# Optimization experiments

Measured on AMD Instinct MI355X. Metric: run time of the kernel, lower is better.

## Reference

```python
import jax, jax.numpy as jnp
import numpy as np

N_IN = 1024
N_OUT = 1024
N_SAMPLES = 64
BATCH = 4096
SIGMA_INITIAL = 0.1
MUMAX_INITIAL = 1.0


def setup_inputs() -> dict:
    key = jax.random.key(0)
    ks = jax.random.split(key, 5)
    lsig = jnp.float32(np.log(SIGMA_INITIAL))
    return {
        "x": jax.random.normal(ks[0], (BATCH, N_IN), dtype=jnp.float32),
        "w_mu": jax.random.uniform(ks[1], (N_OUT, N_IN), dtype=jnp.float32,
                                   minval=-MUMAX_INITIAL, maxval=MUMAX_INITIAL),
        "w_lsigma": jnp.full((N_OUT, N_IN), lsig, dtype=jnp.float32),
        "b_mu": jax.random.uniform(ks[2], (N_OUT,), dtype=jnp.float32,
                                   minval=-MUMAX_INITIAL, maxval=MUMAX_INITIAL),
        "b_lsigma": jnp.full((N_OUT,), lsig, dtype=jnp.float32),
        "r1": jax.random.normal(ks[3], (N_SAMPLES, N_OUT, N_IN), dtype=jnp.float32),
        "r2": jax.random.normal(ks[4], (N_SAMPLES, N_OUT), dtype=jnp.float32),
        "N_samples": N_SAMPLES,
    }


def reference(x, w_mu, w_lsigma, b_mu, b_lsigma, r1, r2, N_samples):
    # Reparameterized weight/bias samples: (S, N_out, N_in), (S, N_out)
    w = w_mu + jnp.exp(w_lsigma) * r1
    b = b_mu + jnp.exp(b_lsigma) * r2
    # y[s, b, o] = sum_i x[b, i] * w[s, o, i] + b[s, o]
    y = jnp.einsum('bi,soi->sbo', x, w) + b[:, None, :]
    return y
```

## Files before the change

### kernel.cpp

```cpp
#include <hip/hip_runtime.h>
#include <hip/hip_bf16.h>
#include <hip/hip_fp8.h>
#include <stdint.h>
#include <type_traits>

#define NIN  1024
#define NOUT 1024
#define NB   4096

typedef float f32x4  __attribute__((ext_vector_type(4)));
typedef float f32x16 __attribute__((ext_vector_type(16)));
typedef __bf16 bf16x8 __attribute__((ext_vector_type(8)));
typedef int   i32x4 __attribute__((ext_vector_type(4)));
typedef int   i32x8 __attribute__((ext_vector_type(8)));

typedef const __attribute__((address_space(1))) unsigned int* gp1_t;
typedef __attribute__((address_space(3))) unsigned int* lp3_t;

__device__ __forceinline__ void gload16(const void* g, void* l) {
    __builtin_amdgcn_global_load_lds((gp1_t)g, (lp3_t)l, 16, 0, 0);
}

__device__ __forceinline__ unsigned short f2bf(float f) {
    __bf16 h = (__bf16)f;
    return __builtin_bit_cast(unsigned short, h);
}

__device__ __forceinline__ unsigned int pk4_fp8(float a, float b, float c, float d) {
#if __has_builtin(__builtin_amdgcn_cvt_pk_fp8_f32)
    int p = __builtin_amdgcn_cvt_pk_fp8_f32(a, b, 0, false);
    p = __builtin_amdgcn_cvt_pk_fp8_f32(c, d, p, true);
    return (unsigned int)p;
#else
    __hip_fp8_e4m3 qa(a), qb(b), qc(c), qd(d);
    return (unsigned int)qa.__x | ((unsigned int)qb.__x << 8) |
           ((unsigned int)qc.__x << 16) | ((unsigned int)qd.__x << 24);
#endif
}

#define BAR   __builtin_amdgcn_s_barrier()
#define LGK0  do { asm volatile("s_waitcnt lgkmcnt(0)" ::: "memory"); __builtin_amdgcn_sched_barrier(0); } while (0)
#define VMW4  do { asm volatile("s_waitcnt vmcnt(4)"  ::: "memory"); __builtin_amdgcn_sched_barrier(0); } while (0)
#define VMW2  do { asm volatile("s_waitcnt vmcnt(2)"  ::: "memory"); __builtin_amdgcn_sched_barrier(0); } while (0)
#define VMW0  do { asm volatile("s_waitcnt vmcnt(0)"  ::: "memory"); __builtin_amdgcn_sched_barrier(0); } while (0)

__global__ void cvt_x_kernel(const float* __restrict__ x, unsigned short* __restrict__ xb) {
    int i = blockIdx.x * blockDim.x + threadIdx.x;
    f32x4 v = reinterpret_cast<const f32x4*>(x)[i];
    ushort4 o;
    o.x = f2bf(v.x); o.y = f2bf(v.y); o.z = f2bf(v.z); o.w = f2bf(v.w);
    reinterpret_cast<ushort4*>(xb)[i] = o;
}

__global__ void cvt_x_fp8(const float* __restrict__ x, unsigned int* __restrict__ xf8) {
    int i = blockIdx.x * blockDim.x + threadIdx.x;
    f32x4 v = reinterpret_cast<const f32x4*>(x)[i];
    xf8[i] = pk4_fp8(v.x, v.y, v.z, v.w);
}

__global__ void cvt_r1_fp8(const float* __restrict__ wls, const float* __restrict__ r1,
                           unsigned int* __restrict__ rf8, int s0) {
    int idx = blockIdx.x * blockDim.x + threadIdx.x;
    int i4 = idx & 262143;
    int c  = idx >> 18;
    f32x4 ls = reinterpret_cast<const f32x4*>(wls)[i4];
    const f32x4* rp = reinterpret_cast<const f32x4*>(r1 + ((size_t)(s0 + c) << 20));
    f32x4 r = __builtin_nontemporal_load(rp + i4);
    rf8[idx] = pk4_fp8(__expf(ls.x) * r.x, __expf(ls.y) * r.y,
                       __expf(ls.z) * r.z, __expf(ls.w) * r.w);
}

__global__ void bias_kernel(const float* __restrict__ bmu, const float* __restrict__ bls,
                            const float* __restrict__ r2, float* __restrict__ bias, int total) {
    int i = blockIdx.x * blockDim.x + threadIdx.x;
    if (i < total) {
        int o = i & (NOUT - 1);
        bias[i] = bmu[o] + __expf(bls[o]) * r2[i];
    }
}

__launch_bounds__(512, 2)
__global__ void gemm256(const unsigned short* __restrict__ xb,
                        const unsigned short* __restrict__ wb,
                        unsigned short* __restrict__ yb, int nwg) {
    __shared__ __align__(16) char smem[131072];
    const int tid = threadIdx.x;
    const int l   = tid & 63;
    const int w   = tid >> 6;
    const int wr  = w >> 2, wc = w & 3;

    const int b   = blockIdx.x;
    const int q8  = nwg >> 3;
    const int g   = (b & 7) * q8 + (b >> 3);
    const int mi  = g & 15;
    const int ni  = g >> 4;
    const int m0  = mi * 256;
    const int n0  = ni * 256;

    const int srow = l >> 3;
    const int scol = ((l & 7) ^ srow) * 8;
    const size_t slane = (size_t)srow * NIN + scol;

    const int rowp  = (l & 15) * 128;
    const int colp0 = ((l >> 4) ^ (l & 7)) << 4;

    f32x4 acc[8][4] = {};
    bf16x8 aF[4][2], b0F[2][2], b1F[2][2];

    const unsigned short* xbase = xb + (size_t)m0 * NIN;
    const unsigned short* wbase = wb + (size_t)n0 * NIN;

    auto STAGE = [&](int buf, int kt, int q) {
        const int R = (q & 3) * 64 + w * 8;
        const unsigned short* src = ((q < 4) ? xbase : wbase)
                                    + (size_t)R * NIN + kt * 64 + slane;
        char* dst = smem + buf * 65536 + ((q >= 4) ? 32768 : 0) + R * 128;
        gload16(src, dst);
    };
    auto LDA = [&](int buf, int mh) {
        const char* base = smem + buf * 65536 + (wr * 128 + mh * 64) * 128 + rowp;
        #pragma unroll
        for (int mb = 0; mb < 4; ++mb) {
            aF[mb][0] = *(const bf16x8*)(base + mb * 2048 + colp0);
            aF[mb][1] = *(const bf16x8*)(base + mb * 2048 + (colp0 ^ 64));
        }
    };
    auto LDB = [&](bf16x8 (&bF)[2][2], int buf, int nh) {
        const char* base = smem + buf * 65536 + 32768 + (wc * 64 + nh * 32) * 128 + rowp;
        #pragma unroll
        for (int nb = 0; nb < 2; ++nb) {
            bF[nb][0] = *(const bf16x8*)(base + nb * 2048 + colp0);
            bF[nb][1] = *(const bf16x8*)(base + nb * 2048 + (colp0 ^ 64));
        }
    };
    auto MM = [&](auto MHc, auto NHc, bf16x8 (&bF)[2][2]) {
        constexpr int MH = decltype(MHc)::value;
        constexpr int NH = decltype(NHc)::value;
        __builtin_amdgcn_s_setprio(1);
        #pragma unroll
        for (int mb = 0; mb < 4; ++mb)
            #pragma unroll
            for (int nb = 0; nb < 2; ++nb)
                #pragma unroll
                for (int kk = 0; kk < 2; ++kk)
                    acc[MH * 4 + mb][NH * 2 + nb] = __builtin_amdgcn_mfma_f32_16x16x32_bf16(
                        aF[mb][kk], bF[nb][kk], acc[MH * 4 + mb][NH * 2 + nb], 0, 0, 0);
        __builtin_amdgcn_s_setprio(0);
    };

    auto C0 = std::integral_constant<int, 0>{};
    auto C1 = std::integral_constant<int, 1>{};

    auto ITER = [&](auto LASTc, int t1, int t2, int t3) {
        constexpr bool LAST = decltype(LASTc)::value;
        LDA(0, 0); LDB(b0F, 0, 0);
        STAGE(1, t1, 2); STAGE(1, t1, 3);
        BAR; LGK0; MM(C0, C0, b0F); BAR;
        LDB(b1F, 0, 1);
        STAGE(1, t1, 4); STAGE(1, t1, 5);
        BAR; LGK0; MM(C0, C1, b1F); BAR;
        LDA(0, 1);
        STAGE(1, t1, 6); STAGE(1, t1, 7);
        BAR; LGK0; MM(C1, C1, b1F); BAR;
        if constexpr (!LAST) { STAGE(0, t2, 0); STAGE(0, t2, 1); }
        BAR; MM(C1, C0, b0F);
        if constexpr (LAST) { VMW0; } else { VMW2; }
        BAR;
        LDA(1, 0); LDB(b0F, 1, 0);
        if constexpr (!LAST) { STAGE(0, t2, 2); STAGE(0, t2, 3); }
        BAR; LGK0; MM(C0, C0, b0F); BAR;
        LDB(b1F, 1, 1);
        if constexpr (!LAST) { STAGE(0, t2, 4); STAGE(0, t2, 5); }
        BAR; LGK0; MM(C0, C1, b1F); BAR;
        LDA(1, 1);
        if constexpr (!LAST) { STAGE(0, t2, 6); STAGE(0, t2, 7); }
        BAR; LGK0; MM(C1, C1, b1F); BAR;
        if constexpr (!LAST) {
            STAGE(1, t3, 0); STAGE(1, t3, 1);
            BAR; MM(C1, C0, b0F); VMW2; BAR;
        } else {
            MM(C1, C0, b0F);
        }
    };

    #pragma unroll
    for (int q = 0; q < 8; ++q) STAGE(0, 0, q);
    STAGE(1, 1, 0); STAGE(1, 1, 1);
    VMW2; BAR;

    #pragma unroll 1
    for (int i = 0; i < 7; ++i)
        ITER(std::false_type{}, 2 * i + 1, 2 * i + 2, 2 * i + 3);
    ITER(std::true_type{}, 15, 16, 17);

    const int oc = n0 + wc * 64 + (l & 15);
    #pragma unroll
    for (int mb = 0; mb < 8; ++mb) {
        #pragma unroll
        for (int i2 = 0; i2 < 4; ++i2) {
            int row = m0 + wr * 128 + mb * 16 + (l >> 4) * 4 + i2;
            unsigned short* rp = yb + (size_t)row * NOUT + oc;
            #pragma unroll
            for (int nb = 0; nb < 4; ++nb)
                rp[nb * 16] = f2bf(acc[mb][nb][i2]);
        }
    }
}

__launch_bounds__(512, 4)
__global__ void gemm_mx(const unsigned char* __restrict__ xf8,
                        const unsigned char* __restrict__ rf8,
                        const unsigned short* __restrict__ y0b,
                        const float* __restrict__ bias,
                        float* __restrict__ out, int s0, int nwg) {
    __shared__ __align__(16) char smem[65536];
    const int tid = threadIdx.x;
    const int l   = tid & 63;
    const int w   = tid >> 6;
    const int wr  = w >> 1, wc = w & 1;

    const int b   = blockIdx.x;
    const int q8  = nwg >> 3;
    const int g   = (b & 7) * q8 + (b >> 3);
    const int nni = nwg >> 5;
    const int mi  = g / nni;
    const int ni  = g - mi * nni;
    const int m0  = mi * 128;
    const int n0  = ni * 128;

    const int srow  = l >> 3;
    const size_t slane = (size_t)srow * NIN + ((l & 7) ^ srow) * 16;

    const int arow = l & 31;
    const int swz  = l & 7;
    const int kx   = (l >> 5) * 2;

    f32x16 acc[2] = {};
    i32x8 aF[2], bF[2][2];

    const unsigned char* xbase = xf8 + (size_t)m0 * NIN;
    const unsigned char* rbase = rf8 + (size_t)n0 * NIN;

    auto STAGE4 = [&](int buf, int t) {
        char* base = smem + buf * 32768;
        #pragma unroll
        for (int q = 0; q < 2; ++q) {
            const int R0 = q * 64 + w * 8;
            gload16(xbase + (size_t)R0 * NIN + t * 128 + slane, base + R0 * 128);
        }
        #pragma unroll
        for (int q = 0; q < 2; ++q) {
            const int R0 = q * 64 + w * 8;
            gload16(rbase + (size_t)R0 * NIN + t * 128 + slane, base + 16384 + R0 * 128);
        }
    };

    auto LDFRAGS = [&](int buf) {
        const char* Ab = smem + buf * 32768;
        const char* rbA = Ab + (wr * 32 + arow) * 128;
        #pragma unroll
        for (int ks = 0; ks < 2; ++ks) {
            int c = ks * 4 + kx;
            i32x4 lo = *(const i32x4*)(rbA + ((c ^ swz) * 16));
            i32x4 hi = *(const i32x4*)(rbA + (((c + 1) ^ swz) * 16));
            aF[ks] = __builtin_shufflevector(lo, hi, 0, 1, 2, 3, 4, 5, 6, 7);
        }
        #pragma unroll
        for (int nb = 0; nb < 2; ++nb) {
            const char* rbB = Ab + 16384 + (wc * 64 + nb * 32 + arow) * 128;
            #pragma unroll
            for (int ks = 0; ks < 2; ++ks) {
                int c = ks * 4 + kx;
                i32x4 lo = *(const i32x4*)(rbB + ((c ^ swz) * 16));
                i32x4 hi = *(const i32x4*)(rbB + (((c + 1) ^ swz) * 16));
                bF[nb][ks] = __builtin_shufflevector(lo, hi, 0, 1, 2, 3, 4, 5, 6, 7);
            }
        }
    };

    STAGE4(0, 0); STAGE4(1, 1);
    VMW4; BAR;

    #pragma unroll 1
    for (int t = 0; t < 8; ++t) {
        const int buf = t & 1;
        LDFRAGS(buf);
        LGK0;
        __builtin_amdgcn_s_setprio(1);
        #pragma unroll
        for (int nb = 0; nb < 2; ++nb)
            #pragma unroll
            for (int ks = 0; ks < 2; ++ks)
                acc[nb] = __builtin_amdgcn_mfma_scale_f32_32x32x64_f8f6f4(
                    aF[ks], bF[nb][ks], acc[nb],
                    0, 0, 0, 127, 0, 127);
        __builtin_amdgcn_s_setprio(0);
        BAR;
        if (t < 6)       { STAGE4(buf, t + 2); VMW4; BAR; }
        else if (t == 6) { VMW0; BAR; }
    }

    BAR;
    const int s   = s0 + (n0 >> 10);
    const int n0c = n0 & 1023;
    float* outp = out + (size_t)s * NB * NOUT;
    float* lds_f = (float*)smem;
    const f32x4 bvv = *(const f32x4*)(bias + (size_t)s * NOUT + n0c + (l & 31) * 4);

    #pragma unroll
    for (int nb = 0; nb < 2; ++nb) {
        const int col = wc * 64 + nb * 32 + (l & 31);
        #pragma unroll
        for (int r = 0; r < 16; ++r) {
            int row = wr * 32 + 4 * (l >> 5) + (r & 3) + 8 * (r >> 2);
            lds_f[row * 128 + col] = acc[nb][r];
        }
    }
    LGK0; BAR;
    #pragma unroll
    for (int k = 0; k < 8; ++k) {
        const int rl  = k * 16 + (tid >> 5);
        const int row = m0 + rl;
        f32x4 v = *(const f32x4*)(lds_f + rl * 128 + (l & 31) * 4);
        ushort4 yu = *(const ushort4*)(y0b + (size_t)row * NOUT + n0c + (l & 31) * 4);
        f32x4 yv;
        yv.x = __builtin_bit_cast(float, (unsigned int)yu.x << 16);
        yv.y = __builtin_bit_cast(float, (unsigned int)yu.y << 16);
        yv.z = __builtin_bit_cast(float, (unsigned int)yu.z << 16);
        yv.w = __builtin_bit_cast(float, (unsigned int)yu.w << 16);
        f32x4 o = v + yv + bvv;
        __builtin_nontemporal_store(o, (f32x4*)(outp + (size_t)row * NOUT + n0c + (l & 31) * 4));
    }
}

__global__ void fused_fallback(const float* __restrict__ x, const float* __restrict__ wmu,
                               const float* __restrict__ wls, const float* __restrict__ r1,
                               const float* __restrict__ bmu, const float* __restrict__ bls,
                               const float* __restrict__ r2, float* __restrict__ out) {
    __shared__ float Xs[16][64];
    __shared__ float Ws[16][64];
    int b0 = blockIdx.x * 16, o0 = blockIdx.y * 16, s = blockIdx.z;
    int tb = threadIdx.x >> 4, to = threadIdx.x & 15;
    float acc = 0.f;
    for (int k0 = 0; k0 < NIN; k0 += 64) {
        __syncthreads();
        #pragma unroll
        for (int j = 0; j < 4; ++j) {
            int e = j * 256 + threadIdx.x;
            int r = e >> 6, cc = e & 63;
            Xs[r][cc] = x[(size_t)(b0 + r) * NIN + k0 + cc];
            size_t wi = (size_t)(o0 + r) * NIN + k0 + cc;
            Ws[r][cc] = wmu[wi] + __expf(wls[wi]) * r1[(size_t)s * NIN * NOUT + wi];
        }
        __syncthreads();
        for (int k = 0; k < 64; ++k) acc += Xs[tb][k] * Ws[to][k];
    }
    int o = o0 + to;
    out[((size_t)s * NB + b0 + tb) * NOUT + o] = acc + bmu[o] + __expf(bls[o]) * r2[s * NOUT + o];
}

extern "C" void kernel_launch(void* const* d_in, const int* in_sizes, int n_in,
                              void* d_out, int out_size, void* d_ws, size_t ws_size,
                              hipStream_t stream) {
    const float* x   = (const float*)d_in[0];
    const float* wmu = (const float*)d_in[1];
    const float* wls = (const float*)d_in[2];
    const float* bmu = (const float*)d_in[3];
    const float* bls = (const float*)d_in[4];
    const float* r1  = (const float*)d_in[5];
    const float* r2  = (const float*)d_in[6];
    const int S = in_sizes[6] / NOUT;
    float* out = (float*)d_out;

    const size_t xb_b   = (size_t)NB * NIN * 2;
    const size_t xf8_b  = (size_t)NB * NIN;
    const size_t wmub_b = (size_t)NOUT * NIN * 2;
    const size_t y0_b   = (size_t)NB * NOUT * 2;
    const size_t bias_b = (size_t)S * NOUT * 4;
    const size_t per_s  = (size_t)NOUT * NIN;
    const size_t base_b = xb_b + xf8_b + wmub_b + y0_b + bias_b;

    if (ws_size < base_b + per_s) {
        dim3 gg(NB / 16, NOUT / 16, S);
        fused_fallback<<<gg, 256, 0, stream>>>(x, wmu, wls, r1, bmu, bls, r2, out);
        return;
    }

    char* ws = (char*)d_ws;
    unsigned short* xb   = (unsigned short*)ws;
    unsigned char*  xf8  = (unsigned char*)(ws + xb_b);
    unsigned short* wmub = (unsigned short*)(ws + xb_b + xf8_b);
    unsigned short* y0b  = (unsigned short*)(ws + xb_b + xf8_b + wmub_b);
    float*          bias = (float*)(ws + xb_b + xf8_b + wmub_b + y0_b);
    unsigned char*  rf8  = (unsigned char*)(ws + base_b);

    int SC = (int)((ws_size - base_b) / per_s);
    if (SC > S) SC = S;

    cvt_x_kernel<<<NB * NIN / 1024, 256, 0, stream>>>(x, xb);
    cvt_x_kernel<<<NOUT * NIN / 1024, 256, 0, stream>>>(wmu, wmub);
    cvt_x_fp8<<<NB * NIN / 1024, 256, 0, stream>>>(x, (unsigned int*)xf8);
    bias_kernel<<<(S * NOUT + 255) / 256, 256, 0, stream>>>(bmu, bls, r2, bias, S * NOUT);

    gemm256<<<64, 512, 0, stream>>>(xb, wmub, y0b, 64);

    for (int s0 = 0; s0 < S; s0 += SC) {
        int sc = (S - s0 < SC) ? (S - s0) : SC;
        cvt_r1_fp8<<<sc * (NOUT * NIN / 1024), 256, 0, stream>>>(wls, r1, (unsigned int*)rf8, s0);
        int nwg = 32 * 8 * sc;
        gemm_mx<<<nwg, 512, 0, stream>>>(xf8, rf8, y0b, bias, out, s0, nwg);
    }
}
```

Measured before the change: 585.5 us.

## Preload y0+bias into accumulators and store directly; fuse x conversion kernels

The FP8 GEMM now initialises its MFMA accumulators from the bf16 mu-GEMM result plus bias before the K loop, then writes the accumulators straight to global memory. This removes the LDS transpose staging, the extra barriers and the separate epilogue reload. The two conversions of x to bf16 and fp8 are merged into one kernel that reads x once. In exchange, the output stores are scalar 4-byte writes strided by row instead of 16-byte vector rows, and the y0 gathers are scalar 2-byte loads. Both may reduce coalescing on a write-bound output of 64x4096x1024 floats.

```diff
diff --git a/kernel.cpp b/kernel.cpp
--- a/kernel.cpp
+++ b/kernel.cpp
@@ -44,18 +44,22 @@
 #define VMW2  do { asm volatile("s_waitcnt vmcnt(2)"  ::: "memory"); __builtin_amdgcn_sched_barrier(0); } while (0)
 #define VMW0  do { asm volatile("s_waitcnt vmcnt(0)"  ::: "memory"); __builtin_amdgcn_sched_barrier(0); } while (0)
 
+__global__ void cvt_x_both(const float* __restrict__ x, unsigned short* __restrict__ xb,
+                           unsigned int* __restrict__ xf8) {
+    int i = blockIdx.x * blockDim.x + threadIdx.x;
+    f32x4 v = reinterpret_cast<const f32x4*>(x)[i];
+    ushort4 o;
+    o.x = f2bf(v.x); o.y = f2bf(v.y); o.z = f2bf(v.z); o.w = f2bf(v.w);
+    reinterpret_cast<ushort4*>(xb)[i] = o;
+    xf8[i] = pk4_fp8(v.x, v.y, v.z, v.w);
+}
+
 __global__ void cvt_x_kernel(const float* __restrict__ x, unsigned short* __restrict__ xb) {
     int i = blockIdx.x * blockDim.x + threadIdx.x;
     f32x4 v = reinterpret_cast<const f32x4*>(x)[i];
     ushort4 o;
     o.x = f2bf(v.x); o.y = f2bf(v.y); o.z = f2bf(v.z); o.w = f2bf(v.w);
     reinterpret_cast<ushort4*>(xb)[i] = o;
-}
-
-__global__ void cvt_x_fp8(const float* __restrict__ x, unsigned int* __restrict__ xf8) {
-    int i = blockIdx.x * blockDim.x + threadIdx.x;
-    f32x4 v = reinterpret_cast<const f32x4*>(x)[i];
-    xf8[i] = pk4_fp8(v.x, v.y, v.z, v.w);
 }
 
 __global__ void cvt_r1_fp8(const float* __restrict__ wls, const float* __restrict__ r1,
@@ -235,11 +239,30 @@
     const int swz  = l & 7;
     const int kx   = (l >> 5) * 2;
 
-    f32x16 acc[2] = {};
+    f32x16 acc[2];
     i32x8 aF[2], bF[2][2];
 
     const unsigned char* xbase = xf8 + (size_t)m0 * NIN;
     const unsigned char* rbase = rf8 + (size_t)n0 * NIN;
+
+    const int s    = s0 + (n0 >> 10);
+    const int n0c  = n0 & 1023;
+    const int colA = n0c + wc * 64 + (l & 31);
+    const int rb0  = m0 + wr * 32 + 4 * (l >> 5);
+    {
+        const float b0v = bias[s * NOUT + colA];
+        const float b1v = bias[s * NOUT + colA + 32];
+        #pragma unroll
+        for (int nb = 0; nb < 2; ++nb)
+            #pragma unroll
+            for (int r = 0; r < 16; ++r) {
+                int row = rb0 + (r & 3) + 8 * (r >> 2);
+                unsigned short u = y0b[(size_t)row * NOUT + colA + nb * 32];
+                acc[nb][r] = __builtin_bit_cast(float, (unsigned int)u << 16)
+                             + (nb ? b1v : b0v);
+            }
+    }
+    __builtin_amdgcn_sched_barrier(0);
 
     auto STAGE4 = [&](int buf, int t) {
         char* base = smem + buf * 32768;
@@ -300,36 +323,15 @@
         else if (t == 6) { VMW0; BAR; }
     }
 
-    BAR;
-    const int s   = s0 + (n0 >> 10);
-    const int n0c = n0 & 1023;
     float* outp = out + (size_t)s * NB * NOUT;
-    float* lds_f = (float*)smem;
-    const f32x4 bvv = *(const f32x4*)(bias + (size_t)s * NOUT + n0c + (l & 31) * 4);
-
     #pragma unroll
     for (int nb = 0; nb < 2; ++nb) {
-        const int col = wc * 64 + nb * 32 + (l & 31);
         #pragma unroll
         for (int r = 0; r < 16; ++r) {
-            int row = wr * 32 + 4 * (l >> 5) + (r & 3) + 8 * (r >> 2);
-            lds_f[row * 128 + col] = acc[nb][r];
-        }
-    }
-    LGK0; BAR;
-    #pragma unroll
-    for (int k = 0; k < 8; ++k) {
-        const int rl  = k * 16 + (tid >> 5);
-        const int row = m0 + rl;
-        f32x4 v = *(const f32x4*)(lds_f + rl * 128 + (l & 31) * 4);
-        ushort4 yu = *(const ushort4*)(y0b + (size_t)row * NOUT + n0c + (l & 31) * 4);
-        f32x4 yv;
-        yv.x = __builtin_bit_cast(float, (unsigned int)yu.x << 16);
-        yv.y = __builtin_bit_cast(float, (unsigned int)yu.y << 16);
-        yv.z = __builtin_bit_cast(float, (unsigned int)yu.z << 16);
-        yv.w = __builtin_bit_cast(float, (unsigned int)yu.w << 16);
-        f32x4 o = v + yv + bvv;
-        __builtin_nontemporal_store(o, (f32x4*)(outp + (size_t)row * NOUT + n0c + (l & 31) * 4));
+            int row = rb0 + (r & 3) + 8 * (r >> 2);
+            __builtin_nontemporal_store(acc[nb][r],
+                outp + (size_t)row * NOUT + colA + nb * 32);
+        }
     }
 }
 
@@ -397,9 +399,8 @@
     int SC = (int)((ws_size - base_b) / per_s);
     if (SC > S) SC = S;
 
-    cvt_x_kernel<<<NB * NIN / 1024, 256, 0, stream>>>(x, xb);
+    cvt_x_both<<<NB * NIN / 1024, 256, 0, stream>>>(x, xb, (unsigned int*)xf8);
     cvt_x_kernel<<<NOUT * NIN / 1024, 256, 0, stream>>>(wmu, wmub);
-    cvt_x_fp8<<<NB * NIN / 1024, 256, 0, stream>>>(x, (unsigned int*)xf8);
     bias_kernel<<<(S * NOUT + 255) / 256, 256, 0, stream>>>(bmu, bls, r2, bias, S * NOUT);
 
     gemm256<<<64, 512, 0, stream>>>(xb, wmub, y0b, 64);
```

Measured after the change: 617.9 us. +5.5%, slower.
